# Performance work log

Hardware: AMD Instinct MI355X
Metric: run time of the kernel (lower is better)

The kernel has to match this reference:

```python
import jax, jax.numpy as jnp
import numpy as np

NUM_TOURS = 200   # fixed segment count (original: tour_index.max()+1)
EPS = 1e-5        # torch InstanceNorm1d default eps


def setup_inputs() -> dict:
    key = jax.random.key(0)
    ks = jax.random.split(key, 9)
    B, P, D = 64, 2000, 128
    embeddings = jax.random.normal(ks[0], (B, P + 1, D), jnp.float32)
    tour_index = jax.random.randint(ks[1], (B, P), 0, NUM_TOURS, dtype=jnp.int32)
    # tour_combiner: Linear(2D -> D); feedforward: Linear(D -> D); stored as (in, out)
    W1 = jax.random.normal(ks[2], (2 * D, D), jnp.float32) / np.sqrt(2 * D)
    b1 = jax.random.normal(ks[3], (D,), jnp.float32) * 0.01
    W2 = jax.random.normal(ks[4], (D, D), jnp.float32) / np.sqrt(D)
    b2 = jax.random.normal(ks[5], (D,), jnp.float32) * 0.01
    # InstanceNorm1d affine params (per channel)
    gamma = 1.0 + 0.1 * jax.random.normal(ks[6], (D,), jnp.float32)
    beta = 0.1 * jax.random.normal(ks[7], (D,), jnp.float32)
    return {
        "batch_size": B, "num_customers": P,
        "tour_index": tour_index, "embeddings": embeddings,
        "W1": W1, "b1": b1, "W2": W2, "b2": b2,
        "gamma": gamma, "beta": beta,
    }


def reference(batch_size, num_customers, tour_index, embeddings, W1, b1, W2, b2, gamma, beta):
    B, P = batch_size, num_customers
    D = embeddings.shape[-1]
    cust = embeddings[:, 1:]                                  # (B, P, D)
    # tour-level segment sum (scatter_add over tour ids, per batch)
    flat_idx = (tour_index + jnp.arange(B, dtype=tour_index.dtype)[:, None] * NUM_TOURS).reshape(-1)
    tour_emb = jax.ops.segment_sum(cust.reshape(B * P, D), flat_idx,
                                   num_segments=B * NUM_TOURS).reshape(B, NUM_TOURS, D)
    # gather tour embedding back to each customer
    cust_tour = jnp.take_along_axis(tour_emb, tour_index[:, :, None], axis=1)  # (B, P, D)
    # concat -> linear -> relu -> linear
    combined = jnp.concatenate([cust, cust_tour], axis=-1)    # (B, P, 2D)
    h = jax.nn.relu(combined @ W1 + b1)
    h = h @ W2 + b2
    # residual + instance norm over the customer axis, per channel
    added = cust + h
    mean = jnp.mean(added, axis=1, keepdims=True)
    var = jnp.var(added, axis=1, keepdims=True)
    normed = (added - mean) * jax.lax.rsqrt(var + EPS) * gamma + beta
    return jnp.concatenate([embeddings[:, :1], normed], axis=1)
```

## Files before the change

### kernel.cpp

```cpp
#include <hip/hip_runtime.h>
#include <stdint.h>

typedef unsigned short u16;
typedef __attribute__((ext_vector_type(8))) short short8;
typedef __attribute__((ext_vector_type(4))) float floatx4;

constexpr int B_ = 64, P_ = 2000, D_ = 128, T_ = 200;

__device__ __forceinline__ u16 f2bf(float f) {
  union { float f; uint32_t u; } v; v.f = f;
  return (u16)((v.u + 0x7fffu + ((v.u >> 16) & 1u)) >> 16);
}

__global__ __launch_bounds__(256) void k_pre(
    const int* __restrict__ tidx, int* __restrict__ list,
    int* __restrict__ goff, int* __restrict__ gcnt,
    const float* __restrict__ W1, const float* __restrict__ W2,
    u16* __restrict__ w1f, u16* __restrict__ w2f, float* __restrict__ ssum) {
  __shared__ int tix[P_];
  __shared__ int cnt[256], scan[256], cur[256];
  const int bid = blockIdx.x, tid = threadIdx.x;

  if (bid >= 64) {
    if (bid < 128) {
      ssum[(bid - 64) * 256 + tid] = 0.f;
      return;
    }
    int t = (bid - 128) * 256 + tid;
    if (t >= 6144) return;
    const float* W = (t < 4096) ? W1 : W2;
    u16* dst = (t < 4096) ? w1f : w2f;
    int fid = (t < 4096) ? t : t - 4096;
    int lane = fid & 63;
    int nt = (fid >> 6) & 7;
    int ks = fid >> 9;
    int quad = lane >> 4, c = lane & 15;
    int k0 = ks * 32 + quad * 8;
#pragma unroll
    for (int j = 0; j < 8; ++j)
      dst[(size_t)fid * 8 + j] = f2bf(W[(k0 + j) * D_ + nt * 16 + c]);
    return;
  }

  const int b = bid;
  cnt[tid] = 0;
  for (int i = tid; i < P_; i += 256) tix[i] = tidx[b * P_ + i];
  __syncthreads();
  for (int i = tid; i < P_; i += 256) atomicAdd(&cnt[tix[i]], 1);
  __syncthreads();
  scan[tid] = cnt[tid];
  __syncthreads();
  for (int s = 1; s < 256; s <<= 1) {
    int v = (tid >= s) ? scan[tid - s] : 0;
    __syncthreads();
    scan[tid] += v;
    __syncthreads();
  }
  int excl = scan[tid] - cnt[tid];
  if (tid < T_) {
    goff[b * T_ + tid] = excl;
    gcnt[b * T_ + tid] = cnt[tid];
  }
  cur[tid] = excl;
  __syncthreads();
  for (int i = tid; i < P_; i += 256) {
    int slot = atomicAdd(&cur[tix[i]], 1);
    list[b * P_ + slot] = i;
  }
}

__global__ __launch_bounds__(256) void k_gather(const float* __restrict__ emb,
                                                const int* __restrict__ list,
                                                const int* __restrict__ goff,
                                                const int* __restrict__ gcnt,
                                                u16* __restrict__ tourb) {
  const int tid = threadIdx.x;
  const int lane = tid & 63, wv = tid >> 6;
  const int seg = blockIdx.x * 4 + wv;
  const int b = seg / T_;
  const int off = goff[seg], cn = gcnt[seg];
  const int* lstb = list + b * P_;
  const float* eb = emb + ((size_t)(b * 2001 + 1)) * D_ + lane * 2;
  float sx = 0.f, sy = 0.f;
  for (int i = 0; i < cn; i += 8) {
    int pr[8];
#pragma unroll
    for (int j = 0; j < 8; ++j)
      if (i + j < cn) pr[j] = lstb[off + i + j];
    float2 v[8];
#pragma unroll
    for (int j = 0; j < 8; ++j)
      if (i + j < cn) v[j] = *(const float2*)(eb + (size_t)pr[j] * D_);
#pragma unroll
    for (int j = 0; j < 8; ++j)
      if (i + j < cn) { sx += v[j].x; sy += v[j].y; }
  }
  uint32_t pk = (uint32_t)f2bf(sx) | ((uint32_t)f2bf(sy) << 16);
  ((uint32_t*)(tourb + (size_t)seg * D_))[lane] = pk;
}

__global__ __launch_bounds__(256, 6) void k_mlp(
    const int* __restrict__ tidx, const float* __restrict__ emb,
    const u16* __restrict__ tourb,
    const u16* __restrict__ w1f, const u16* __restrict__ w2f,
    const float* __restrict__ b1, const float* __restrict__ b2,
    float* __restrict__ ssum, float* __restrict__ ssq,
    float* __restrict__ out) {
  __shared__ u16 hbuf[64 * 136];
  __shared__ float red[2][2][128];
  const int tid = threadIdx.x;
  const int w = tid >> 6, lane = tid & 63, quad = lane >> 4, c = lane & 15;
  const int base = blockIdx.x * 64;
  const int r0 = w * 16;

  for (int i = tid; i < 512; i += 256) ((float*)red)[i] = 0.f;

  const int blo = base / P_;
  const int bhi = (base + 63) / P_;
  const bool straddle = (blo != bhi);
  const int bsplit = bhi * P_;

  const int m0 = base + r0 + c;
  const int ab = m0 / P_, ap = m0 - ab * P_;
  const float* arow = emb + ((size_t)(ab * 2001 + 1 + ap)) * D_;
  const u16* trow = tourb + ((size_t)(ab * T_ + tidx[m0])) * D_;

  float bias1[8], bias2[8];
#pragma unroll
  for (int nt = 0; nt < 8; ++nt) {
    bias1[nt] = b1[nt * 16 + c];
    bias2[nt] = b2[nt * 16 + c];
  }

  floatx4 acc[8];
#pragma unroll
  for (int nt = 0; nt < 8; ++nt) acc[nt] = (floatx4)0.f;

#pragma unroll
  for (int ks = 0; ks < 8; ++ks) {
    short8 a;
    if (ks < 4) {
      const float* src = arow + ks * 32 + quad * 8;
      floatx4 x0 = *(const floatx4*)src;
      floatx4 x1 = *(const floatx4*)(src + 4);
#pragma unroll
      for (int j = 0; j < 4; ++j) {
        a[j]     = (short)f2bf(x0[j]);
        a[4 + j] = (short)f2bf(x1[j]);
      }
    } else {
      a = *(const short8*)(trow + (ks - 4) * 32 + quad * 8);
    }
#pragma unroll
    for (int nt = 0; nt < 8; ++nt) {
      short8 bf = *(const short8*)(w1f + ((size_t)((ks * 8 + nt) * 64 + lane)) * 8);
      acc[nt] = __builtin_amdgcn_mfma_f32_16x16x32_bf16(a, bf, acc[nt], 0, 0, 0);
    }
  }

#pragma unroll
  for (int nt = 0; nt < 8; ++nt)
#pragma unroll
    for (int r = 0; r < 4; ++r) {
      int row = r0 + quad * 4 + r;
      float v = acc[nt][r] + bias1[nt];
      hbuf[row * 136 + nt * 16 + c] = f2bf(v > 0.f ? v : 0.f);
    }
  __syncthreads();

  floatx4 acc2[8];
#pragma unroll
  for (int nt = 0; nt < 8; ++nt) acc2[nt] = (floatx4)0.f;

#pragma unroll
  for (int ks = 0; ks < 4; ++ks) {
    short8 a = *(const short8*)(&hbuf[(r0 + c) * 136 + ks * 32 + quad * 8]);
#pragma unroll
    for (int nt = 0; nt < 8; ++nt) {
      short8 bf = *(const short8*)(w2f + ((size_t)((ks * 8 + nt) * 64 + lane)) * 8);
      acc2[nt] = __builtin_amdgcn_mfma_f32_16x16x32_bf16(a, bf, acc2[nt], 0, 0, 0);
    }
  }

  float s[8], q[8];
#pragma unroll
  for (int nt = 0; nt < 8; ++nt) { s[nt] = 0.f; q[nt] = 0.f; }
#pragma unroll
  for (int nt = 0; nt < 8; ++nt)
#pragma unroll
    for (int r = 0; r < 4; ++r) {
      int row = r0 + quad * 4 + r;
      int m = base + row;
      int b = m / P_, p = m - b * P_;
      size_t gaddr = ((size_t)(b * 2001 + 1 + p)) * D_ + nt * 16 + c;
      float v = emb[gaddr] + (acc2[nt][r] + bias2[nt]);
      out[gaddr] = v;
      if (!straddle || m < bsplit) {
        s[nt] += v; q[nt] += v * v;
      } else {
        atomicAdd(&red[1][0][nt * 16 + c], v);
        atomicAdd(&red[1][1][nt * 16 + c], v * v);
      }
    }
#pragma unroll
  for (int nt = 0; nt < 8; ++nt) {
    s[nt] += __shfl_xor(s[nt], 16);
    s[nt] += __shfl_xor(s[nt], 32);
    q[nt] += __shfl_xor(q[nt], 16);
    q[nt] += __shfl_xor(q[nt], 32);
  }
  if (quad == 0) {
#pragma unroll
    for (int nt = 0; nt < 8; ++nt) {
      atomicAdd(&red[0][0][nt * 16 + c], s[nt]);
      atomicAdd(&red[0][1][nt * 16 + c], q[nt]);
    }
  }
  __syncthreads();
  if (tid < 128) {
    atomicAdd(&ssum[blo * D_ + tid], red[0][0][tid]);
    if (straddle) atomicAdd(&ssum[bhi * D_ + tid], red[1][0][tid]);
  } else {
    int col = tid - 128;
    atomicAdd(&ssq[blo * D_ + col], red[0][1][col]);
    if (straddle) atomicAdd(&ssq[bhi * D_ + col], red[1][1][col]);
  }
}

__global__ __launch_bounds__(256) void k_out(
    const float* __restrict__ emb,
    const float* __restrict__ ssum, const float* __restrict__ ssq,
    const float* __restrict__ gamma, const float* __restrict__ beta,
    float* __restrict__ out) {
  size_t i = ((size_t)blockIdx.x * 256 + threadIdx.x) * 8;
  int row = (int)(i >> 7), col = (int)(i & 127);
  int b = row / 2001, r = row - b * 2001;
  if (r == 0) {
    *(floatx4*)(out + i)     = *(const floatx4*)(emb + i);
    *(floatx4*)(out + i + 4) = *(const floatx4*)(emb + i + 4);
  } else {
    floatx4 a0 = *(const floatx4*)(out + i);
    floatx4 a1 = *(const floatx4*)(out + i + 4);
    int cc = b * D_ + col;
    floatx4 su0 = *(const floatx4*)(ssum + cc);
    floatx4 su1 = *(const floatx4*)(ssum + cc + 4);
    floatx4 sq0 = *(const floatx4*)(ssq + cc);
    floatx4 sq1 = *(const floatx4*)(ssq + cc + 4);
    floatx4 g0  = *(const floatx4*)(gamma + col);
    floatx4 g1  = *(const floatx4*)(gamma + col + 4);
    floatx4 be0 = *(const floatx4*)(beta + col);
    floatx4 be1 = *(const floatx4*)(beta + col + 4);
    constexpr float invP = 1.f / P_;
#pragma unroll
    for (int j = 0; j < 4; ++j) {
      float mean = su0[j] * invP;
      float var  = sq0[j] * invP - mean * mean;
      float sc   = rsqrtf(var + 1e-5f) * g0[j];
      a0[j] = a0[j] * sc + (be0[j] - mean * sc);
      float mean1 = su1[j] * invP;
      float var1  = sq1[j] * invP - mean1 * mean1;
      float sc1   = rsqrtf(var1 + 1e-5f) * g1[j];
      a1[j] = a1[j] * sc1 + (be1[j] - mean1 * sc1);
    }
    *(floatx4*)(out + i)     = a0;
    *(floatx4*)(out + i + 4) = a1;
  }
}

extern "C" void kernel_launch(void* const* d_in, const int* in_sizes, int n_in,
                              void* d_out, int out_size, void* d_ws, size_t ws_size,
                              hipStream_t stream) {
  const int*   tour_index = (const int*)d_in[2];
  const float* emb   = (const float*)d_in[3];
  const float* W1    = (const float*)d_in[4];
  const float* b1    = (const float*)d_in[5];
  const float* W2    = (const float*)d_in[6];
  const float* b2    = (const float*)d_in[7];
  const float* gamma = (const float*)d_in[8];
  const float* beta  = (const float*)d_in[9];
  float* out = (float*)d_out;
  char* ws = (char*)d_ws;

  u16*   w1f   = (u16*)(ws);
  u16*   w2f   = (u16*)(ws + 65536);
  float* ssum  = (float*)(ws + 98304);
  float* ssq   = ssum + B_ * D_;
  u16*   tourb = (u16*)(ws + 229376);
  int*   list  = (int*)(ws + 3506176);
  int*   goff  = (int*)(ws + 4018176);
  int*   gcnt  = (int*)(ws + 4069376);

  hipLaunchKernelGGL(k_pre,    dim3(152),  dim3(256), 0, stream,
                     tour_index, list, goff, gcnt, W1, W2, w1f, w2f, ssum);
  hipLaunchKernelGGL(k_gather, dim3(3200), dim3(256), 0, stream, emb, list, goff, gcnt, tourb);
  hipLaunchKernelGGL(k_mlp,    dim3(2000), dim3(256), 0, stream, tour_index, emb, tourb,
                     w1f, w2f, b1, b2, ssum, ssq, out);
  hipLaunchKernelGGL(k_out,    dim3(8004), dim3(256), 0, stream, emb, ssum, ssq, gamma, beta, out);
}
```

Baseline: 244.0 us.

## Stage MLP weights through double-buffered LDS with async global_load_lds prefetch

In k_mlp, each wave previously read W1/W2 fragments straight from global memory. Now each k-slice of weights is staged into a double-buffered LDS tile with global_load_lds, with the next slice prefetched while MFMAs run on the current one. The activation and tour rows are loaded up front, and the residual embedding values are prefetched before the second GEMM. The cost is more LDS, a barrier per k-step, more registers, and launch bounds lowered from 6 to 4 waves per SIMD, which can reduce occupancy.

```diff
diff --git a/kernel.cpp b/kernel.cpp
--- a/kernel.cpp
+++ b/kernel.cpp
@@ -10,6 +10,12 @@
 __device__ __forceinline__ u16 f2bf(float f) {
   union { float f; uint32_t u; } v; v.f = f;
   return (u16)((v.u + 0x7fffu + ((v.u >> 16) & 1u)) >> 16);
+}
+
+__device__ __forceinline__ void g2lds16(const void* g, void* l) {
+  __builtin_amdgcn_global_load_lds(
+      (const __attribute__((address_space(1))) uint32_t*)g,
+      (__attribute__((address_space(3))) uint32_t*)l, 16, 0, 0);
 }
 
 __global__ __launch_bounds__(256) void k_pre(
@@ -99,13 +105,14 @@
   ((uint32_t*)(tourb + (size_t)seg * D_))[lane] = pk;
 }
 
-__global__ __launch_bounds__(256, 6) void k_mlp(
+__global__ __launch_bounds__(256, 4) void k_mlp(
     const int* __restrict__ tidx, const float* __restrict__ emb,
     const u16* __restrict__ tourb,
     const u16* __restrict__ w1f, const u16* __restrict__ w2f,
     const float* __restrict__ b1, const float* __restrict__ b2,
     float* __restrict__ ssum, float* __restrict__ ssq,
     float* __restrict__ out) {
+  __shared__ u16 wbuf[2][4096];
   __shared__ u16 hbuf[64 * 136];
   __shared__ float red[2][2][128];
   const int tid = threadIdx.x;
@@ -125,6 +132,21 @@
   const float* arow = emb + ((size_t)(ab * 2001 + 1 + ap)) * D_;
   const u16* trow = tourb + ((size_t)(ab * T_ + tidx[m0])) * D_;
 
+  g2lds16(w1f + (size_t)tid * 8,        (u16*)wbuf[0] + (size_t)tid * 8);
+  g2lds16(w1f + 2048 + (size_t)tid * 8, (u16*)wbuf[0] + 2048 + (size_t)tid * 8);
+
+  floatx4 xa[4][2];
+#pragma unroll
+  for (int ks = 0; ks < 4; ++ks) {
+    const float* src = arow + ks * 32 + quad * 8;
+    xa[ks][0] = *(const floatx4*)src;
+    xa[ks][1] = *(const floatx4*)(src + 4);
+  }
+  short8 ta[4];
+#pragma unroll
+  for (int ks = 0; ks < 4; ++ks)
+    ta[ks] = *(const short8*)(trow + ks * 32 + quad * 8);
+
   float bias1[8], bias2[8];
 #pragma unroll
   for (int nt = 0; nt < 8; ++nt) {
@@ -136,37 +158,56 @@
 #pragma unroll
   for (int nt = 0; nt < 8; ++nt) acc[nt] = (floatx4)0.f;
 
+  __syncthreads();
+
 #pragma unroll
   for (int ks = 0; ks < 8; ++ks) {
+    const int cur = ks & 1;
+    if (ks < 7) {
+      const u16* src = w1f + (size_t)(ks + 1) * 4096;
+      g2lds16(src + (size_t)tid * 8,        (u16*)wbuf[cur ^ 1] + (size_t)tid * 8);
+      g2lds16(src + 2048 + (size_t)tid * 8, (u16*)wbuf[cur ^ 1] + 2048 + (size_t)tid * 8);
+    } else {
+      g2lds16(w2f + (size_t)tid * 8,        (u16*)wbuf[0] + (size_t)tid * 8);
+      g2lds16(w2f + 2048 + (size_t)tid * 8, (u16*)wbuf[0] + 2048 + (size_t)tid * 8);
+    }
     short8 a;
     if (ks < 4) {
-      const float* src = arow + ks * 32 + quad * 8;
-      floatx4 x0 = *(const floatx4*)src;
-      floatx4 x1 = *(const floatx4*)(src + 4);
 #pragma unroll
       for (int j = 0; j < 4; ++j) {
-        a[j]     = (short)f2bf(x0[j]);
-        a[4 + j] = (short)f2bf(x1[j]);
+        a[j]     = (short)f2bf(xa[ks][0][j]);
+        a[4 + j] = (short)f2bf(xa[ks][1][j]);
       }
     } else {
-      a = *(const short8*)(trow + (ks - 4) * 32 + quad * 8);
+      a = ta[ks - 4];
     }
 #pragma unroll
     for (int nt = 0; nt < 8; ++nt) {
-      short8 bf = *(const short8*)(w1f + ((size_t)((ks * 8 + nt) * 64 + lane)) * 8);
+      short8 bf = *(const short8*)(&wbuf[cur][(nt * 64 + lane) * 8]);
       acc[nt] = __builtin_amdgcn_mfma_f32_16x16x32_bf16(a, bf, acc[nt], 0, 0, 0);
     }
-  }
-
+    if (ks == 7) {
+#pragma unroll
+      for (int nt = 0; nt < 8; ++nt)
+#pragma unroll
+        for (int r = 0; r < 4; ++r) {
+          int row = r0 + quad * 4 + r;
+          float v = acc[nt][r] + bias1[nt];
+          hbuf[row * 136 + nt * 16 + c] = f2bf(v > 0.f ? v : 0.f);
+        }
+    }
+    __syncthreads();
+  }
+
+  float eemb[8][4];
 #pragma unroll
   for (int nt = 0; nt < 8; ++nt)
 #pragma unroll
     for (int r = 0; r < 4; ++r) {
-      int row = r0 + quad * 4 + r;
-      float v = acc[nt][r] + bias1[nt];
-      hbuf[row * 136 + nt * 16 + c] = f2bf(v > 0.f ? v : 0.f);
-    }
-  __syncthreads();
+      int m = base + r0 + quad * 4 + r;
+      int b = m / P_, p = m - b * P_;
+      eemb[nt][r] = emb[((size_t)(b * 2001 + 1 + p)) * D_ + nt * 16 + c];
+    }
 
   floatx4 acc2[8];
 #pragma unroll
@@ -174,12 +215,19 @@
 
 #pragma unroll
   for (int ks = 0; ks < 4; ++ks) {
+    const int cur = ks & 1;
+    if (ks < 3) {
+      const u16* src = w2f + (size_t)(ks + 1) * 4096;
+      g2lds16(src + (size_t)tid * 8,        (u16*)wbuf[cur ^ 1] + (size_t)tid * 8);
+      g2lds16(src + 2048 + (size_t)tid * 8, (u16*)wbuf[cur ^ 1] + 2048 + (size_t)tid * 8);
+    }
     short8 a = *(const short8*)(&hbuf[(r0 + c) * 136 + ks * 32 + quad * 8]);
 #pragma unroll
     for (int nt = 0; nt < 8; ++nt) {
-      short8 bf = *(const short8*)(w2f + ((size_t)((ks * 8 + nt) * 64 + lane)) * 8);
+      short8 bf = *(const short8*)(&wbuf[cur][(nt * 64 + lane) * 8]);
       acc2[nt] = __builtin_amdgcn_mfma_f32_16x16x32_bf16(a, bf, acc2[nt], 0, 0, 0);
     }
+    if (ks < 3) __syncthreads();
   }
 
   float s[8], q[8];
@@ -193,7 +241,7 @@
       int m = base + row;
       int b = m / P_, p = m - b * P_;
       size_t gaddr = ((size_t)(b * 2001 + 1 + p)) * D_ + nt * 16 + c;
-      float v = emb[gaddr] + (acc2[nt][r] + bias2[nt]);
+      float v = eemb[nt][r] + (acc2[nt][r] + bias2[nt]);
       out[gaddr] = v;
       if (!straddle || m < bsplit) {
         s[nt] += v; q[nt] += v * v;
```

Result: faster. 211.7 us (-13.2%).
